# Performance work log

Hardware: AMD Instinct MI355X
Metric: run time of the kernel (lower is better)

Reference implementation:

```python
import jax, jax.numpy as jnp
import numpy as np

ALPHA = 0.2  # LeakyReLU negative slope
MASK_VAL = -9e15


def setup_inputs() -> dict:
    key = jax.random.key(0)
    k1, k2, k3, k4 = jax.random.split(key, 4)
    B, N, F_IN = 4, 2048, 256
    H, HD = 8, 32  # out_features = H*HD = 256
    x = jax.random.normal(k1, (B, N, F_IN), dtype=jnp.float32)
    adj = jax.random.randint(k2, (B, N, N), 0, 2, dtype=jnp.int32)
    W = jax.random.normal(k3, (H, F_IN, HD), dtype=jnp.float32) * (1.0 / np.sqrt(F_IN))
    a = jax.random.normal(k4, (H, 2 * HD, 1), dtype=jnp.float32) * 0.1
    return {"x": x, "adj": adj, "W": W, "a": a}


def reference(x, adj, W, a):
    # x: (B,N,F), W: (H,F,D), a: (H,2D,1)
    B, N, _ = x.shape
    H, _, D = W.shape
    Wh = jnp.einsum('bnf,hfd->bhnd', x, W)  # (B,H,N,D)
    # Split additive attention vector: cat([Wh_i, Wh_j]) @ a == Wh_i@a1 + Wh_j@a2
    a1 = a[:, :D, 0]   # (H,D)
    a2 = a[:, D:, 0]   # (H,D)
    s1 = jnp.einsum('bhnd,hd->bhn', Wh, a1)  # source scores
    s2 = jnp.einsum('bhnd,hd->bhn', Wh, a2)  # target scores
    e = jax.nn.leaky_relu(s1[:, :, :, None] + s2[:, :, None, :], negative_slope=ALPHA)  # (B,H,N,N)
    e = jnp.where(adj[:, None, :, :] == 0, MASK_VAL, e)
    attention = jax.nn.softmax(e, axis=-1)  # dropout skipped (eval mode)
    h = jnp.einsum('bhij,bhjd->bhid', attention, Wh)  # (B,H,N,D)
    h = jnp.transpose(h, (0, 2, 1, 3)).reshape(B, N, H * D)
    return jax.nn.elu(h)
```

## Files before the change

### kernel.cpp

```cpp
#include <hip/hip_runtime.h>
#include <hip/hip_bf16.h>

#define ALPHA 0.2f

typedef __attribute__((ext_vector_type(8))) short short8;
typedef __attribute__((ext_vector_type(4))) short s4;
typedef __attribute__((ext_vector_type(8))) _Float16 h8;
typedef __attribute__((ext_vector_type(2))) _Float16 h2v;
typedef __attribute__((ext_vector_type(4))) float f32x4;
typedef __attribute__((ext_vector_type(2))) short sh2;

static constexpr int B = 4, N = 2048, F = 256, H = 8, D = 32;
static constexpr int SZ_X = B * N * F, SZ_ADJ = B * N * N, SZ_W = H * F * D, SZ_A = H * 2 * D;
static const float C1 = 1.4426950408889634f;
static const float C2 = ALPHA * 1.4426950408889634f;


__device__ __forceinline__ unsigned rne16(unsigned u) {
    return u + 0x7fffu + ((u >> 16) & 1u);
}
__device__ __forceinline__ unsigned pk_rne(float a, float b) {
    return __builtin_amdgcn_perm(rne16(__float_as_uint(b)),
                                 rne16(__float_as_uint(a)), 0x07060302u);
}
__device__ __forceinline__ unsigned h2mul(unsigned a, unsigned b) {
    h2v r = __builtin_bit_cast(h2v, a) * __builtin_bit_cast(h2v, b);
    return __builtin_bit_cast(unsigned, r);
}
__device__ __forceinline__ unsigned h2max(unsigned a, unsigned b) {
    h2v r = __builtin_elementwise_max(__builtin_bit_cast(h2v, a),
                                      __builtin_bit_cast(h2v, b));
    return __builtin_bit_cast(unsigned, r);
}
__device__ __forceinline__ unsigned dup16f(float x) {
    unsigned short w = __builtin_bit_cast(unsigned short, (_Float16)x);
    return (unsigned)w | ((unsigned)w << 16);
}
__device__ __forceinline__ unsigned bits2mask(unsigned mk, unsigned mulc) {
    unsigned w = (mk & 3u) * mulc;
    sh2 s = __builtin_bit_cast(sh2, w);
    s = s >> 15;
    return __builtin_bit_cast(unsigned, s);
}

__global__ void k0_prep(const float* __restrict__ Wp, const float* __restrict__ ap,
                        unsigned short* __restrict__ WT2, float* __restrict__ AF) {
    int bid = blockIdx.x;
    int h = bid >> 5, d = bid & 31;
    int f = threadIdx.x;
    unsigned short v = (unsigned short)(rne16(__float_as_uint(Wp[(h * F + f) * D + d])) >> 16);
    WT2[(size_t)(f >> 5) * 8192 + (h * 32 + d) * 32 + (f & 31)] = v;
    if (d == 0 && f < 64) AF[h * 64 + f] = ap[h * 64 + f];
}

__global__ __launch_bounds__(256, 4) void k2_fused(const float* __restrict__ x,
                                                   const unsigned short* __restrict__ WT2,
                                                   const float* __restrict__ AF,
                                                   unsigned short* __restrict__ WHT,
                                                   float* __restrict__ S1,
                                                   _Float16* __restrict__ UH,
                                                   _Float16* __restrict__ VH,
                                                   const int* __restrict__ adj,
                                                   unsigned long long* __restrict__ bm) {
    __shared__ unsigned short XA[16 * 264];
    int bid = blockIdx.x;
    int rr = bid % 5;
    int grp = bid / 5;
    int t = threadIdx.x;

    if (rr != 4) {
        int wid = (grp * 4 + rr) * 4 + (t >> 6);
        int lane = t & 63;
        size_t base = (size_t)wid * 32;
        const int* ap2 = adj + base * 64 + lane;
        int v0[16], v1[16];
#pragma unroll
        for (int s = 0; s < 16; s++) v0[s] = ap2[(size_t)s * 64];
#pragma unroll
        for (int s = 0; s < 16; s++) v1[s] = ap2[(size_t)(16 + s) * 64];
        unsigned long long m0[16];
#pragma unroll
        for (int s = 0; s < 16; s++) m0[s] = __ballot(v0[s] != 0);
        unsigned long long m1[16];
#pragma unroll
        for (int s = 0; s < 16; s++) m1[s] = __ballot(v1[s] != 0);
        if (lane == 0) {
#pragma unroll
            for (int s = 0; s < 16; s++) bm[base + s] = m0[s];
#pragma unroll
            for (int s = 0; s < 16; s++) bm[base + 16 + s] = m1[s];
        }
        return;
    }

    int b = grp >> 7;
    int n0 = (grp & 127) * 16;
    int wave = t >> 6, lane = t & 63;
    int lm = lane & 15, lq = lane >> 4;

#pragma unroll
    for (int q = 0; q < 4; q++) {
        int idx = q * 256 + t;
        int row = idx >> 6, c16 = idx & 63;
        f32x4 v = *(const f32x4*)(x + (size_t)(b * N + n0 + row) * F + c16 * 4);
        unsigned* dst = (unsigned*)&XA[row * 264 + c16 * 4];
        dst[0] = pk_rne(v[0], v[1]);
        dst[1] = pk_rne(v[2], v[3]);
    }

    short8 bcur[4], bnext[4];
#pragma unroll
    for (int c = 0; c < 4; c++)
        bcur[c] = *(const short8*)(WT2 + (size_t)(wave * 64 + c * 16 + lm) * 32 + lq * 8);
    __syncthreads();

    f32x4 acc[4] = {};
#pragma unroll
    for (int kc = 0; kc < 8; kc++) {
        if (kc < 7) {
#pragma unroll
            for (int c = 0; c < 4; c++)
                bnext[c] = *(const short8*)(WT2 + (size_t)(kc + 1) * 8192 +
                                            (wave * 64 + c * 16 + lm) * 32 + lq * 8);
        }
        short8 afr = *(const short8*)&XA[lm * 264 + kc * 32 + lq * 8];
#pragma unroll
        for (int c = 0; c < 4; c++)
            acc[c] = __builtin_amdgcn_mfma_f32_16x16x32_bf16(afr, bcur[c], acc[c], 0, 0, 0);
#pragma unroll
        for (int c = 0; c < 4; c++) bcur[c] = bnext[c];
    }

#pragma unroll
    for (int c = 0; c < 4; c++) {
        int hd = wave * 64 + c * 16 + lm;
        unsigned short w0 = __builtin_bit_cast(unsigned short, (_Float16)acc[c][0]);
        unsigned short w1 = __builtin_bit_cast(unsigned short, (_Float16)acc[c][1]);
        unsigned short w2 = __builtin_bit_cast(unsigned short, (_Float16)acc[c][2]);
        unsigned short w3 = __builtin_bit_cast(unsigned short, (_Float16)acc[c][3]);
        uint2 pk;
        pk.x = (unsigned)w0 | ((unsigned)w1 << 16);
        pk.y = (unsigned)w2 | ((unsigned)w3 << 16);
        *(uint2*)&WHT[((size_t)b * 256 + hd) * 2048 + n0 + lq * 4] = pk;
    }
#pragma unroll
    for (int cp = 0; cp < 2; cp++) {
        int h = wave * 2 + cp;
        float a1l = AF[h * 64 + lm],      a1h = AF[h * 64 + 16 + lm];
        float a2l = AF[h * 64 + 32 + lm], a2h = AF[h * 64 + 48 + lm];
#pragma unroll
        for (int r = 0; r < 4; r++) {
            float s1p = acc[cp * 2][r] * a1l + acc[cp * 2 + 1][r] * a1h;
            float s2p = acc[cp * 2][r] * a2l + acc[cp * 2 + 1][r] * a2h;
#pragma unroll
            for (int off = 1; off <= 8; off <<= 1) {
                s1p += __shfl_xor(s1p, off);
                s2p += __shfl_xor(s2p, off);
            }
            if (lm == 0) {
                int bh = b * 8 + h, n = n0 + lq * 4 + r;
                S1[(size_t)bh * 2048 + n] = s1p;
                UH[(size_t)bh * 2048 + n] = (_Float16)exp2f(C1 * s2p);
                VH[(size_t)bh * 2048 + n] = (_Float16)exp2f(C2 * s2p);
            }
        }
    }
}

__global__ __launch_bounds__(256) void k3_attn(
    const unsigned* __restrict__ bm32,
    const unsigned short* __restrict__ WHT,
    const float* __restrict__ S1,
    const _Float16* __restrict__ UH, const _Float16* __restrict__ VH,
    float* __restrict__ out) {
    __shared__ unsigned LM[4][16 * 68];
    __shared__ unsigned short LW[4][32 * 140];

    int bid = blockIdx.x;
    int bh = (bid & 7) + ((bid >> 8) << 3);
    int tile = (bid >> 3) & 31;
    int b = bh >> 3, h = bh & 7;
    int i0 = tile * 64;
    int t = threadIdx.x;
    int wave = t >> 6, lane = t & 63;
    int irow = lane & 15, quad = lane >> 4;
    int iw = i0 + wave * 16;

    {
        unsigned* lmp = LM[wave];
        const unsigned* src = bm32 + ((size_t)(b * N + iw)) * 64;
#pragma unroll
        for (int r = 0; r < 16; r++)
            lmp[r * 68 + lane] = src[(size_t)r * 64 + lane];
    }

    const unsigned short* wsrc = WHT + ((size_t)b * 256 + h * 32) * 2048;
    int srow = t >> 3, sseg = (t & 7) * 16;

    {
        const unsigned short* g0 = wsrc + (size_t)srow * 2048 + sseg;
        union { short8 v; s4 q[2]; } a0, c0, a1, c1;
        a0.v = *(const short8*)(g0);
        c0.v = *(const short8*)(g0 + 8);
        a1.v = *(const short8*)(g0 + 128);
        c1.v = *(const short8*)(g0 + 136);
        unsigned short* d0 = &LW[0][srow * 140 + sseg];
        *(s4*)(d0) = a0.q[0]; *(s4*)(d0 + 4) = a0.q[1];
        *(s4*)(d0 + 8) = c0.q[0]; *(s4*)(d0 + 12) = c0.q[1];
        unsigned short* d1 = &LW[1][srow * 140 + sseg];
        *(s4*)(d1) = a1.q[0]; *(s4*)(d1 + 4) = a1.q[1];
        *(s4*)(d1 + 8) = c1.q[0]; *(s4*)(d1 + 12) = c1.q[1];
    }

    float s1A = S1[(size_t)bh * 2048 + iw + irow];
    unsigned ci2A = dup16f(exp2f((C2 - C1) * s1A));
    const _Float16* up = UH + (size_t)bh * 2048;
    const _Float16* vp = VH + (size_t)bh * 2048;

    union { h8 v; unsigned u[4]; } ones;
    ones.u[0] = ones.u[1] = ones.u[2] = ones.u[3] = 0x3C003C00u;

    const unsigned MUL = 0x40008000u;

    f32x4 aA0 = {0,0,0,0}, aA1 = {0,0,0,0}, aAL = {0,0,0,0};
    __syncthreads();

    for (int g = 0; g < 8; g++) {
        union { short8 v; s4 q[2]; } pa0, pc0, pa1, pc1;
        if (g < 7) {
            const unsigned short* g0 = wsrc + (size_t)srow * 2048 + (2 * g + 2) * 128 + sseg;
            pa0.v = *(const short8*)(g0);
            pc0.v = *(const short8*)(g0 + 8);
            pa1.v = *(const short8*)(g0 + 128);
            pc1.v = *(const short8*)(g0 + 136);
        }
        const unsigned* lmw = LM[wave];
#pragma unroll
        for (int ci = 0; ci < 2; ci++) {
            int cc = 2 * g + ci;
            const unsigned short* lwp = LW[cc & 3];
            uint4 mkq = *(const uint4*)&lmw[irow * 68 + cc * 4];
            unsigned mkw[4] = { mkq.x, mkq.y, mkq.z, mkq.w };
            uint4 uws[4], vws[4];
#pragma unroll
            for (int ks = 0; ks < 4; ks++) {
                uws[ks] = *(const uint4*)(up + cc * 128 + ks * 32 + quad * 8);
                vws[ks] = *(const uint4*)(vp + cc * 128 + ks * 32 + quad * 8);
            }
#pragma unroll
            for (int ks = 0; ks < 4; ks++) {
                int jl = ks * 32 + quad * 8;
                unsigned mkA = mkw[ks] >> (quad * 8);
                unsigned mA0 = bits2mask(mkA,      MUL);
                unsigned mA1 = bits2mask(mkA >> 2, MUL);
                unsigned mA2 = bits2mask(mkA >> 4, MUL);
                unsigned mA3 = bits2mask(mkA >> 6, MUL);
                union { h8 v; unsigned u[4]; } afA;
                afA.u[0] = h2max(uws[ks].x, h2mul(ci2A, vws[ks].x)) & mA0;
                afA.u[1] = h2max(uws[ks].y, h2mul(ci2A, vws[ks].y)) & mA1;
                afA.u[2] = h2max(uws[ks].z, h2mul(ci2A, vws[ks].z)) & mA2;
                afA.u[3] = h2max(uws[ks].w, h2mul(ci2A, vws[ks].w)) & mA3;
                union { short8 v; s4 q[2]; } bf0, bf1;
                bf0.q[0] = *(const s4*)&lwp[irow * 140 + jl];
                bf0.q[1] = *(const s4*)&lwp[irow * 140 + jl + 4];
                bf1.q[0] = *(const s4*)&lwp[(16 + irow) * 140 + jl];
                bf1.q[1] = *(const s4*)&lwp[(16 + irow) * 140 + jl + 4];
                h8 b0 = __builtin_bit_cast(h8, bf0.v);
                h8 b1 = __builtin_bit_cast(h8, bf1.v);
                aA0 = __builtin_amdgcn_mfma_f32_16x16x32_f16(afA.v, b0, aA0, 0, 0, 0);
                aA1 = __builtin_amdgcn_mfma_f32_16x16x32_f16(afA.v, b1, aA1, 0, 0, 0);
                aAL = __builtin_amdgcn_mfma_f32_16x16x32_f16(afA.v, ones.v, aAL, 0, 0, 0);
            }
        }
        if (g < 7) {
            unsigned short* d0 = &LW[(2 * g + 2) & 3][srow * 140 + sseg];
            *(s4*)(d0) = pa0.q[0]; *(s4*)(d0 + 4) = pa0.q[1];
            *(s4*)(d0 + 8) = pc0.q[0]; *(s4*)(d0 + 12) = pc0.q[1];
            unsigned short* d1 = &LW[(2 * g + 3) & 3][srow * 140 + sseg];
            *(s4*)(d1) = pa1.q[0]; *(s4*)(d1 + 4) = pa1.q[1];
            *(s4*)(d1 + 8) = pc1.q[0]; *(s4*)(d1 + 12) = pc1.q[1];
        }
        __syncthreads();
    }

#pragma unroll
    for (int r = 0; r < 4; r++) {
        float lA = aAL[r];
        float rA = 1.0f / (lA > 0.f ? lA : 1.f);
        float vA0 = aA0[r] * rA, vA1 = aA1[r] * rA;
        vA0 = vA0 > 0.f ? vA0 : __expf(vA0) - 1.f;
        vA1 = vA1 > 0.f ? vA1 : __expf(vA1) - 1.f;
        int iA = iw + quad * 4 + r;
        size_t rbA = (size_t)(b * N + iA) * 256 + h * 32;
        out[rbA + irow] = vA0;
        out[rbA + 16 + irow] = vA1;
    }
}

extern "C" void kernel_launch(void* const* d_in, const int* in_sizes, int n_in,
                              void* d_out, int out_size, void* d_ws, size_t ws_size,
                              hipStream_t stream) {
    const void *xP = nullptr, *adjP = nullptr, *WP = nullptr, *aP = nullptr;
    for (int i = 0; i < n_in; i++) {
        switch (in_sizes[i]) {
            case SZ_X:   xP = d_in[i]; break;
            case SZ_ADJ: adjP = d_in[i]; break;
            case SZ_W:   WP = d_in[i]; break;
            case SZ_A:   aP = d_in[i]; break;
            default: break;
        }
    }
    if (!xP || !adjP || !WP || !aP) { xP = d_in[0]; adjP = d_in[1]; WP = d_in[2]; aP = d_in[3]; }
    float* out = (float*)d_out;

    char* ws = (char*)d_ws;
    unsigned short* WT2 = (unsigned short*)(ws);
    float* AF  = (float*)(ws + 131072);
    float* S1  = (float*)(ws + 133120);
    _Float16* UH = (_Float16*)(ws + 395264);
    _Float16* VH = (_Float16*)(ws + 526336);
    unsigned short* WHT = (unsigned short*)(ws + 657408);
    unsigned long long* BM = (unsigned long long*)(ws + 4851712);

    k0_prep<<<256, 256, 0, stream>>>((const float*)WP, (const float*)aP, WT2, AF);
    k2_fused<<<2560, 256, 0, stream>>>((const float*)xP, WT2, AF, WHT, S1, UH, VH,
                                       (const int*)adjP, BM);
    k3_attn<<<1024, 256, 0, stream>>>((const unsigned*)BM, WHT, S1, UH, VH, out);
}
```

Baseline: 146.8 us.

## Double attention block to 128 rows with 512 threads sharing WH tiles

The attention kernel now uses 512-thread blocks covering 128 query rows (8 waves) instead of 64, so each staged WH^T chunk in LDS is reused by twice as many waves. The cooperative load is spread over twice as many threads, each moving half as much data. Loads of the U/V vectors are moved inside the ks loop to lower register pressure, and launch bounds request 4 blocks per CU. The grid halves, which costs parallelism and raises LDS use per block.

```diff
diff --git a/kernel.cpp b/kernel.cpp
--- a/kernel.cpp
+++ b/kernel.cpp
@@ -167,20 +167,20 @@
     }
 }
 
-__global__ __launch_bounds__(256) void k3_attn(
+__global__ __launch_bounds__(512, 4) void k3_attn(
     const unsigned* __restrict__ bm32,
     const unsigned short* __restrict__ WHT,
     const float* __restrict__ S1,
     const _Float16* __restrict__ UH, const _Float16* __restrict__ VH,
     float* __restrict__ out) {
-    __shared__ unsigned LM[4][16 * 68];
+    __shared__ unsigned LM[8][16 * 68];
     __shared__ unsigned short LW[4][32 * 140];
 
     int bid = blockIdx.x;
-    int bh = (bid & 7) + ((bid >> 8) << 3);
-    int tile = (bid >> 3) & 31;
+    int bh = (bid & 7) + ((bid >> 7) << 3);
+    int isup = (bid >> 3) & 15;
     int b = bh >> 3, h = bh & 7;
-    int i0 = tile * 64;
+    int i0 = isup * 128;
     int t = threadIdx.x;
     int wave = t >> 6, lane = t & 63;
     int irow = lane & 15, quad = lane >> 4;
@@ -195,21 +195,17 @@
     }
 
     const unsigned short* wsrc = WHT + ((size_t)b * 256 + h * 32) * 2048;
-    int srow = t >> 3, sseg = (t & 7) * 16;
+    int srow = t >> 4, sseg = (t & 15) * 8;
 
     {
         const unsigned short* g0 = wsrc + (size_t)srow * 2048 + sseg;
-        union { short8 v; s4 q[2]; } a0, c0, a1, c1;
+        union { short8 v; s4 q[2]; } a0, a1;
         a0.v = *(const short8*)(g0);
-        c0.v = *(const short8*)(g0 + 8);
         a1.v = *(const short8*)(g0 + 128);
-        c1.v = *(const short8*)(g0 + 136);
         unsigned short* d0 = &LW[0][srow * 140 + sseg];
         *(s4*)(d0) = a0.q[0]; *(s4*)(d0 + 4) = a0.q[1];
-        *(s4*)(d0 + 8) = c0.q[0]; *(s4*)(d0 + 12) = c0.q[1];
         unsigned short* d1 = &LW[1][srow * 140 + sseg];
         *(s4*)(d1) = a1.q[0]; *(s4*)(d1 + 4) = a1.q[1];
-        *(s4*)(d1 + 8) = c1.q[0]; *(s4*)(d1 + 12) = c1.q[1];
     }
 
     float s1A = S1[(size_t)bh * 2048 + iw + irow];
@@ -226,13 +222,11 @@
     __syncthreads();
 
     for (int g = 0; g < 8; g++) {
-        union { short8 v; s4 q[2]; } pa0, pc0, pa1, pc1;
+        union { short8 v; s4 q[2]; } pa0, pa1;
         if (g < 7) {
             const unsigned short* g0 = wsrc + (size_t)srow * 2048 + (2 * g + 2) * 128 + sseg;
             pa0.v = *(const short8*)(g0);
-            pc0.v = *(const short8*)(g0 + 8);
             pa1.v = *(const short8*)(g0 + 128);
-            pc1.v = *(const short8*)(g0 + 136);
         }
         const unsigned* lmw = LM[wave];
 #pragma unroll
@@ -241,25 +235,22 @@
             const unsigned short* lwp = LW[cc & 3];
             uint4 mkq = *(const uint4*)&lmw[irow * 68 + cc * 4];
             unsigned mkw[4] = { mkq.x, mkq.y, mkq.z, mkq.w };
-            uint4 uws[4], vws[4];
-#pragma unroll
-            for (int ks = 0; ks < 4; ks++) {
-                uws[ks] = *(const uint4*)(up + cc * 128 + ks * 32 + quad * 8);
-                vws[ks] = *(const uint4*)(vp + cc * 128 + ks * 32 + quad * 8);
-            }
 #pragma unroll
             for (int ks = 0; ks < 4; ks++) {
                 int jl = ks * 32 + quad * 8;
+                int jg = cc * 128 + jl;
+                uint4 uw = *(const uint4*)(up + jg);
+                uint4 vw = *(const uint4*)(vp + jg);
                 unsigned mkA = mkw[ks] >> (quad * 8);
                 unsigned mA0 = bits2mask(mkA,      MUL);
                 unsigned mA1 = bits2mask(mkA >> 2, MUL);
                 unsigned mA2 = bits2mask(mkA >> 4, MUL);
                 unsigned mA3 = bits2mask(mkA >> 6, MUL);
                 union { h8 v; unsigned u[4]; } afA;
-                afA.u[0] = h2max(uws[ks].x, h2mul(ci2A, vws[ks].x)) & mA0;
-                afA.u[1] = h2max(uws[ks].y, h2mul(ci2A, vws[ks].y)) & mA1;
-                afA.u[2] = h2max(uws[ks].z, h2mul(ci2A, vws[ks].z)) & mA2;
-                afA.u[3] = h2max(uws[ks].w, h2mul(ci2A, vws[ks].w)) & mA3;
+                afA.u[0] = h2max(uw.x, h2mul(ci2A, vw.x)) & mA0;
+                afA.u[1] = h2max(uw.y, h2mul(ci2A, vw.y)) & mA1;
+                afA.u[2] = h2max(uw.z, h2mul(ci2A, vw.z)) & mA2;
+                afA.u[3] = h2max(uw.w, h2mul(ci2A, vw.w)) & mA3;
                 union { short8 v; s4 q[2]; } bf0, bf1;
                 bf0.q[0] = *(const s4*)&lwp[irow * 140 + jl];
                 bf0.q[1] = *(const s4*)&lwp[irow * 140 + jl + 4];
@@ -275,10 +266,8 @@
         if (g < 7) {
             unsigned short* d0 = &LW[(2 * g + 2) & 3][srow * 140 + sseg];
             *(s4*)(d0) = pa0.q[0]; *(s4*)(d0 + 4) = pa0.q[1];
-            *(s4*)(d0 + 8) = pc0.q[0]; *(s4*)(d0 + 12) = pc0.q[1];
             unsigned short* d1 = &LW[(2 * g + 3) & 3][srow * 140 + sseg];
             *(s4*)(d1) = pa1.q[0]; *(s4*)(d1 + 4) = pa1.q[1];
-            *(s4*)(d1 + 8) = pc1.q[0]; *(s4*)(d1 + 12) = pc1.q[1];
         }
         __syncthreads();
     }
@@ -325,5 +314,5 @@
     k0_prep<<<256, 256, 0, stream>>>((const float*)WP, (const float*)aP, WT2, AF);
     k2_fused<<<2560, 256, 0, stream>>>((const float*)xP, WT2, AF, WHT, S1, UH, VH,
                                        (const int*)adjP, BM);
-    k3_attn<<<1024, 256, 0, stream>>>((const unsigned*)BM, WHT, S1, UH, VH, out);
-}
+    k3_attn<<<512, 512, 0, stream>>>((const unsigned*)BM, WHT, S1, UH, VH, out);
+}
```

Result: no change. 146.0 us (-0.5%).
